# Kernel tuning notes

Hardware: AMD Instinct MI355X
Metric: run time of the kernel (lower is better)

The kernel has to match this reference:

```python
import jax, jax.numpy as jnp
import numpy as np

NUM_LEVELS = 16
F_PER_LEVEL = 2
LOG2_T = 19
TABLE_SIZE = 1 << LOG2_T  # 524288 entries per level
BASE_RES = 16
DESIRED_RES = 4096
PER_LEVEL_SCALE = np.exp(np.log(DESIRED_RES / BASE_RES) / (NUM_LEVELS - 1))
PRIMES = (np.uint32(1), np.uint32(2654435761), np.uint32(805459861))
N_POINTS = 4_194_304

# 8 corner offsets of the trilinear cell, bit i of corner index -> dim offset
_CORNERS = jnp.array([[(i >> d) & 1 for d in range(3)] for i in range(8)], dtype=jnp.float32)  # [8,3]


def hashgrid_encode(texc, table):
    """texc: [N,3] in [0,1]; table: [L, T, F]. Returns [N, L*F] (tcnn HashGrid math)."""
    feats = []
    for lvl in range(NUM_LEVELS):
        scale = float(np.exp2(lvl * np.log2(PER_LEVEL_SCALE)) * BASE_RES - 1.0)
        res = int(np.ceil(scale)) + 1
        pos = texc * scale + 0.5                    # [N,3]
        pg = jnp.floor(pos)
        frac = pos - pg                             # [N,3]
        corner = pg[:, None, :] + _CORNERS[None]    # [N,8,3]
        ci = corner.astype(jnp.uint32)
        # trilinear weights: prod over dims of frac (offset=1) or 1-frac (offset=0)
        w = jnp.prod(jnp.where(_CORNERS[None] == 1.0, frac[:, None, :], 1.0 - frac[:, None, :]), axis=-1)  # [N,8]
        if res ** 3 <= TABLE_SIZE:
            # dense level: index = x + y*res + z*res^2
            idx = ci[..., 0] + ci[..., 1] * jnp.uint32(res) + ci[..., 2] * jnp.uint32(res * res)
        else:
            # hashed level: spatial hash with xor of per-dim primes, mod 2^19
            idx = (ci[..., 0] * PRIMES[0]) ^ (ci[..., 1] * PRIMES[1]) ^ (ci[..., 2] * PRIMES[2])
            idx = idx & jnp.uint32(TABLE_SIZE - 1)
        g = table[lvl][idx.astype(jnp.int32)]       # [N,8,F] irregular gather
        feats.append(jnp.einsum('nc,ncf->nf', w, g))
    return jnp.concatenate(feats, axis=-1)          # [N, 32]


def setup_inputs() -> dict:
    key = jax.random.key(0)
    k0, k1, k2, k3, k4 = jax.random.split(key, 5)
    texc = jax.random.uniform(k0, (N_POINTS, 3), dtype=jnp.float32)
    # tcnn inits hashgrid params uniform in [-1e-4, 1e-4]
    table = (jax.random.uniform(k1, (NUM_LEVELS, TABLE_SIZE, F_PER_LEVEL), dtype=jnp.float32) * 2.0 - 1.0) * 1e-4
    # kaiming_uniform (relu) bound = sqrt(6/fan_in)
    def kaiming(k, shape):
        bound = float(np.sqrt(6.0 / shape[1]))
        return jax.random.uniform(k, shape, dtype=jnp.float32, minval=-bound, maxval=bound)
    W0 = kaiming(k2, (32, 32))
    W1 = kaiming(k3, (32, 32))
    W2 = kaiming(k4, (3, 32))
    return {"texc": texc, "table": table, "W0": W0, "W1": W1, "W2": W2}


def reference(texc, table, W0, W1, W2):
    enc = hashgrid_encode(texc, table)              # [N,32]
    h = jax.nn.relu(enc @ W0.T)
    h = jax.nn.relu(h @ W1.T)
    out = jax.nn.sigmoid(h @ W2.T)                  # [N,3]
    return out
```

## Files before the change

### kernel.cpp

```cpp
#include <hip/hip_runtime.h>
#include <math.h>

#define NUM_LEVELS 16
#define N_DENSE 5
#define N_HASH (NUM_LEVELS - N_DENSE)
#define TABLE_SIZE (1u << 19)
#define TMASK (TABLE_SIZE - 1u)

typedef float f32x4 __attribute__((ext_vector_type(4)));
typedef float f32x2 __attribute__((ext_vector_type(2)));
typedef short s16x8 __attribute__((ext_vector_type(8)));
typedef unsigned u32x2 __attribute__((ext_vector_type(2)));
typedef unsigned u32x4 __attribute__((ext_vector_type(4)));

struct HashParams { float scale[N_HASH]; };
struct DenseParams { float scale[N_DENSE]; unsigned res[N_DENSE]; };
struct AllParams { float scale[NUM_LEVELS]; unsigned res[NUM_LEVELS]; };

static __device__ __forceinline__ unsigned bf16_bits(float f) {
    const unsigned u = __builtin_bit_cast(unsigned, f);
    return (u + (0x7fffu + ((u >> 16) & 1u))) >> 16;
}
static __device__ __forceinline__ short bf16s(float f) { return (short)bf16_bits(f); }
static __device__ __forceinline__ float bflo(unsigned v) { return __builtin_bit_cast(float, v << 16); }
static __device__ __forceinline__ float bfhi(unsigned v) { return __builtin_bit_cast(float, v & 0xffff0000u); }

static __device__ __forceinline__ s16x8 packW8(const float* __restrict__ p) {
    const f32x4 a = *(const f32x4*)p;
    const f32x4 b = *(const f32x4*)(p + 4);
    s16x8 v;
    v[0] = bf16s(a.x); v[1] = bf16s(a.y); v[2] = bf16s(a.z); v[3] = bf16s(a.w);
    v[4] = bf16s(b.x); v[5] = bf16s(b.y); v[6] = bf16s(b.z); v[7] = bf16s(b.w);
    return v;
}
static __device__ __forceinline__ s16x8 packW8sig(const float* __restrict__ row, int q) {
    const f32x4 lo = *(const f32x4*)(row + 4 * q);
    const f32x4 hi = *(const f32x4*)(row + 16 + 4 * q);
    s16x8 v;
    v[0] = bf16s(lo.x); v[1] = bf16s(hi.x); v[2] = bf16s(lo.y); v[3] = bf16s(hi.y);
    v[4] = bf16s(lo.z); v[5] = bf16s(hi.z); v[6] = bf16s(lo.w); v[7] = bf16s(hi.w);
    return v;
}

__global__ __launch_bounds__(256) void cvt_table_kernel(
    const f32x4* __restrict__ src, u32x2* __restrict__ dst, int n2)
{
    const int i = blockIdx.x * 256 + threadIdx.x;
    if (i >= n2) return;
    const f32x4 g = __builtin_nontemporal_load(src + i);
    u32x2 o;
    o.x = bf16_bits(g.x) | (bf16_bits(g.y) << 16);
    o.y = bf16_bits(g.z) | (bf16_bits(g.w) << 16);
    dst[i] = o;
}

template <bool BT>
__global__ __launch_bounds__(256) void hashed_all_kernel(
    const float* __restrict__ texc,
    const float* __restrict__ tf,
    const unsigned* __restrict__ tb,
    unsigned* __restrict__ enc_ws,
    int n, int B, HashParams P)
{
    __shared__ float tst[768];
    const int tid = threadIdx.x;
    const unsigned lvl = blockIdx.x / (unsigned)B;
    const unsigned blk = blockIdx.x - lvl * (unsigned)B;
    const int i0 = (int)blk * 256;

    tst[tid]       = __builtin_nontemporal_load(texc + 3 * i0 + tid);
    tst[tid + 256] = __builtin_nontemporal_load(texc + 3 * i0 + tid + 256);
    tst[tid + 512] = __builtin_nontemporal_load(texc + 3 * i0 + tid + 512);
    __syncthreads();

    const float s = P.scale[lvl];
    const float tx = tst[3 * tid + 0], ty = tst[3 * tid + 1], tz = tst[3 * tid + 2];

    const float px = tx * s + 0.5f, py = ty * s + 0.5f, pz = tz * s + 0.5f;
    const float gx = floorf(px), gy = floorf(py), gz = floorf(pz);
    const float wx = px - gx, wy = py - gy, wz = pz - gz;
    const unsigned x0 = (unsigned)gx, y0 = (unsigned)gy, z0 = (unsigned)gz;

    const unsigned hy0 = y0 * 2654435761u, hy1 = (y0 + 1u) * 2654435761u;
    const unsigned hz0 = z0 * 805459861u,  hz1 = (z0 + 1u) * 805459861u;
    const unsigned hh[4] = { hy0 ^ hz0, hy1 ^ hz0, hy0 ^ hz1, hy1 ^ hz1 };
    const float wyz[4] = { (1.f - wy) * (1.f - wz), wy * (1.f - wz),
                           (1.f - wy) * wz,         wy * wz };
    const float wx0 = 1.f - wx, wx1 = wx;

    float f0 = 0.f, f1 = 0.f;

    if constexpr (BT) {
        const unsigned* tbl = tb + ((size_t)(N_DENSE + lvl) << 19);
        if ((x0 & 1u) == 0u) {
#pragma unroll
            for (int c = 0; c < 4; ++c) {
                const unsigned idx0 = (x0 ^ hh[c]) & TMASK;
                const u32x2 g = *(const u32x2*)(tbl + (idx0 & ~1u));
                const bool sw = (idx0 & 1u) != 0u;
                const unsigned ea = sw ? g.y : g.x;
                const unsigned eb = sw ? g.x : g.y;
                f0 += wyz[c] * (wx0 * bflo(ea) + wx1 * bflo(eb));
                f1 += wyz[c] * (wx0 * bfhi(ea) + wx1 * bfhi(eb));
            }
        } else {
#pragma unroll
            for (int c = 0; c < 4; ++c) {
                const unsigned ea = tbl[(x0 ^ hh[c]) & TMASK];
                const unsigned eb = tbl[((x0 + 1u) ^ hh[c]) & TMASK];
                f0 += wyz[c] * (wx0 * bflo(ea) + wx1 * bflo(eb));
                f1 += wyz[c] * (wx0 * bfhi(ea) + wx1 * bfhi(eb));
            }
        }
    } else {
        const float* tbl = tf + ((size_t)(N_DENSE + lvl) << 20);
        if ((x0 & 1u) == 0u) {
#pragma unroll
            for (int c = 0; c < 4; ++c) {
                const unsigned idx0 = (x0 ^ hh[c]) & TMASK;
                const f32x4 g = *(const f32x4*)(tbl + 2 * (size_t)(idx0 & ~1u));
                const bool hi = (idx0 & 1u) != 0u;
                const float g0x = hi ? g.z : g.x, g0y = hi ? g.w : g.y;
                const float g1x = hi ? g.x : g.z, g1y = hi ? g.y : g.w;
                f0 += wyz[c] * (wx0 * g0x + wx1 * g1x);
                f1 += wyz[c] * (wx0 * g0y + wx1 * g1y);
            }
        } else {
#pragma unroll
            for (int c = 0; c < 4; ++c) {
                const unsigned ia = (x0 ^ hh[c]) & TMASK;
                const unsigned ib = ((x0 + 1u) ^ hh[c]) & TMASK;
                const f32x2 ga = *(const f32x2*)(tbl + 2 * (size_t)ia);
                const f32x2 gb = *(const f32x2*)(tbl + 2 * (size_t)ib);
                f0 += wyz[c] * (wx0 * ga.x + wx1 * gb.x);
                f1 += wyz[c] * (wx0 * ga.y + wx1 * gb.y);
            }
        }
    }

    const unsigned packed = bf16_bits(f0) | (bf16_bits(f1) << 16);
    __builtin_nontemporal_store(packed, enc_ws + (size_t)lvl * n + (i0 + tid));
}

template <bool BT>
__global__ __launch_bounds__(256) void dense_mlp_kernel(
    const float* __restrict__ texc,
    const float* __restrict__ tf,
    const unsigned* __restrict__ tb,
    const unsigned* __restrict__ enc_ws,
    const float* __restrict__ W0,
    const float* __restrict__ W1,
    const float* __restrict__ W2,
    float* __restrict__ out,
    int n, DenseParams P)
{
    __shared__ float tst[768];
    __shared__ __align__(16) unsigned char slabs[4 * 64 * 80];
    const int tid = threadIdx.x;
    const int i0 = blockIdx.x * 256;

    tst[tid]       = __builtin_nontemporal_load(texc + 3 * i0 + tid);
    tst[tid + 256] = __builtin_nontemporal_load(texc + 3 * i0 + tid + 256);
    tst[tid + 512] = __builtin_nontemporal_load(texc + 3 * i0 + tid + 512);
    __syncthreads();

    const int i = i0 + tid;
    unsigned dd[16];

#pragma unroll
    for (int l = 0; l < N_HASH; ++l)
        dd[N_DENSE + l] = __builtin_nontemporal_load(enc_ws + (size_t)l * n + i);

    const float tx = tst[3 * tid + 0], ty = tst[3 * tid + 1], tz = tst[3 * tid + 2];

#pragma unroll
    for (int l = 0; l < N_DENSE; ++l) {
        const float s = P.scale[l];
        const unsigned res = P.res[l];
        const unsigned res2 = res * res;
        const float px = tx * s + 0.5f, py = ty * s + 0.5f, pz = tz * s + 0.5f;
        const float gx = floorf(px), gy = floorf(py), gz = floorf(pz);
        const float wx = px - gx, wy = py - gy, wz = pz - gz;
        const unsigned x0 = (unsigned)gx, y0 = (unsigned)gy, z0 = (unsigned)gz;
        const float wx0 = 1.f - wx, wx1 = wx;
        const float wyz[4] = { (1.f - wy) * (1.f - wz), wy * (1.f - wz),
                               (1.f - wy) * wz,         wy * wz };
        const unsigned base[4] = { y0 * res + z0 * res2, (y0 + 1u) * res + z0 * res2,
                                   y0 * res + (z0 + 1u) * res2,
                                   (y0 + 1u) * res + (z0 + 1u) * res2 };
        float f0 = 0.f, f1 = 0.f;
        if constexpr (BT) {
            const unsigned* tbl = tb + ((size_t)l << 19);
#pragma unroll
            for (int c = 0; c < 4; ++c) {
                const unsigned idx0 = x0 + base[c];
                unsigned ea, eb;
                if ((idx0 & 1u) == 0u) {
                    const u32x2 g = *(const u32x2*)(tbl + idx0);
                    ea = g.x; eb = g.y;
                } else {
                    ea = tbl[idx0]; eb = tbl[idx0 + 1u];
                }
                f0 += wyz[c] * (wx0 * bflo(ea) + wx1 * bflo(eb));
                f1 += wyz[c] * (wx0 * bfhi(ea) + wx1 * bfhi(eb));
            }
        } else {
            const float* tbl = tf + ((size_t)l << 20);
#pragma unroll
            for (int c = 0; c < 4; ++c) {
                const unsigned idx0 = x0 + base[c];
                if ((idx0 & 1u) == 0u) {
                    const f32x4 g = *(const f32x4*)(tbl + 2 * (size_t)idx0);
                    f0 += wyz[c] * (wx0 * g.x + wx1 * g.z);
                    f1 += wyz[c] * (wx0 * g.y + wx1 * g.w);
                } else {
                    const f32x2 ga = *(const f32x2*)(tbl + 2 * (size_t)idx0);
                    const f32x2 gb = *(const f32x2*)(tbl + 2 * (size_t)(idx0 + 1u));
                    f0 += wyz[c] * (wx0 * ga.x + wx1 * gb.x);
                    f1 += wyz[c] * (wx0 * ga.y + wx1 * gb.y);
                }
            }
        }
        dd[l] = bf16_bits(f0) | (bf16_bits(f1) << 16);
    }

    const int lane = tid & 63;
    const int wv = tid >> 6;
    const int c16 = lane & 15, q = lane >> 4;
    unsigned char* slabB = slabs + wv * (64 * 80);
    unsigned* slab = (unsigned*)slabB;

    *(u32x4*)(slabB + lane * 80 +  0) = (u32x4){ dd[0],  dd[1],  dd[2],  dd[3]  };
    *(u32x4*)(slabB + lane * 80 + 16) = (u32x4){ dd[4],  dd[5],  dd[6],  dd[7]  };
    *(u32x4*)(slabB + lane * 80 + 32) = (u32x4){ dd[8],  dd[9],  dd[10], dd[11] };
    *(u32x4*)(slabB + lane * 80 + 48) = (u32x4){ dd[12], dd[13], dd[14], dd[15] };

    const s16x8 b00 = packW8(W0 + c16 * 32 + 8 * q);
    const s16x8 b01 = packW8(W0 + (16 + c16) * 32 + 8 * q);
    const s16x8 b10 = packW8sig(W1 + c16 * 32, q);
    const s16x8 b11 = packW8sig(W1 + (16 + c16) * 32, q);
    const f32x4 zero4 = { 0.f, 0.f, 0.f, 0.f };

    f32x4 d0[4][2];
#pragma unroll
    for (int t = 0; t < 4; ++t) {
        const s16x8 a = *(const s16x8*)(slabB + (16 * t + c16) * 80 + 16 * q);
        d0[t][0] = __builtin_amdgcn_mfma_f32_16x16x32_bf16(a, b00, zero4, 0, 0, 0);
        d0[t][1] = __builtin_amdgcn_mfma_f32_16x16x32_bf16(a, b01, zero4, 0, 0, 0);
    }
#pragma unroll
    for (int t = 0; t < 4; ++t)
#pragma unroll
        for (int r = 0; r < 4; ++r) {
            const unsigned pk = bf16_bits(fmaxf(d0[t][0][r], 0.f)) |
                                (bf16_bits(fmaxf(d0[t][1][r], 0.f)) << 16);
            slab[(16 * t + 4 * q + r) * 20 + c16] = pk;
        }

    f32x4 d1[4][2];
#pragma unroll
    for (int t = 0; t < 4; ++t) {
        const s16x8 a = *(const s16x8*)(slabB + (16 * t + c16) * 80 + 16 * q);
        d1[t][0] = __builtin_amdgcn_mfma_f32_16x16x32_bf16(a, b10, zero4, 0, 0, 0);
        d1[t][1] = __builtin_amdgcn_mfma_f32_16x16x32_bf16(a, b11, zero4, 0, 0, 0);
    }
#pragma unroll
    for (int t = 0; t < 4; ++t)
#pragma unroll
        for (int r = 0; r < 4; ++r) {
            const unsigned pk = bf16_bits(fmaxf(d1[t][0][r], 0.f)) |
                                (bf16_bits(fmaxf(d1[t][1][r], 0.f)) << 16);
            slab[(16 * t + 4 * q + r) * 20 + c16] = pk;
        }

    float z0 = 0.f, z1 = 0.f, z2 = 0.f;
#pragma unroll
    for (int d = 0; d < 16; ++d) {
        const unsigned v = slab[lane * 20 + d];
        const float a0 = bflo(v), a1 = bfhi(v);
        z0 = fmaf(a0, W2[0 * 32 + d], fmaf(a1, W2[0 * 32 + 16 + d], z0));
        z1 = fmaf(a0, W2[1 * 32 + d], fmaf(a1, W2[1 * 32 + 16 + d], z1));
        z2 = fmaf(a0, W2[2 * 32 + d], fmaf(a1, W2[2 * 32 + 16 + d], z2));
    }
    out[3 * i + 0] = 1.f / (1.f + __expf(-z0));
    out[3 * i + 1] = 1.f / (1.f + __expf(-z1));
    out[3 * i + 2] = 1.f / (1.f + __expf(-z2));
}

__global__ __launch_bounds__(256) void mono_kernel(
    const float* __restrict__ texc, const float* __restrict__ table,
    const float* __restrict__ W0, const float* __restrict__ W1,
    const float* __restrict__ W2, float* __restrict__ out, int n, AllParams p)
{
    int i = blockIdx.x * 256 + threadIdx.x;
    if (i >= n) return;
    const float tx = texc[3 * i], ty = texc[3 * i + 1], tz = texc[3 * i + 2];
    float enc[2 * NUM_LEVELS];
#pragma unroll
    for (int l = 0; l < NUM_LEVELS; ++l) {
        const float s = p.scale[l];
        const unsigned res = p.res[l];
        const float px = tx * s + 0.5f, py = ty * s + 0.5f, pz = tz * s + 0.5f;
        const float gx = floorf(px), gy = floorf(py), gz = floorf(pz);
        const float wx = px - gx, wy = py - gy, wz = pz - gz;
        const unsigned x0 = (unsigned)gx, y0 = (unsigned)gy, z0 = (unsigned)gz;
        const float2* tbl = (const float2*)(table + ((size_t)l << 20));
        float f0 = 0.f, f1 = 0.f;
#pragma unroll
        for (int c = 0; c < 8; ++c) {
            const unsigned dx = c & 1u, dy = (c >> 1) & 1u, dz = (c >> 2) & 1u;
            const unsigned xi = x0 + dx, yi = y0 + dy, zi = z0 + dz;
            unsigned idx;
            if (l < N_DENSE) idx = xi + yi * res + zi * res * res;
            else idx = (xi ^ (yi * 2654435761u) ^ (zi * 805459861u)) & TMASK;
            const float2 g = tbl[idx];
            const float w = (dx ? wx : 1.f - wx) * (dy ? wy : 1.f - wy) *
                            (dz ? wz : 1.f - wz);
            f0 = fmaf(w, g.x, f0);
            f1 = fmaf(w, g.y, f1);
        }
        enc[2 * l] = f0;
        enc[2 * l + 1] = f1;
    }
    float h1[32];
#pragma unroll
    for (int j = 0; j < 32; ++j) {
        float acc = 0.f;
#pragma unroll
        for (int k = 0; k < 32; ++k) acc = fmaf(enc[k], W0[j * 32 + k], acc);
        h1[j] = fmaxf(acc, 0.f);
    }
    float h2[32];
#pragma unroll
    for (int j = 0; j < 32; ++j) {
        float acc = 0.f;
#pragma unroll
        for (int k = 0; k < 32; ++k) acc = fmaf(h1[k], W1[j * 32 + k], acc);
        h2[j] = fmaxf(acc, 0.f);
    }
#pragma unroll
    for (int j = 0; j < 3; ++j) {
        float acc = 0.f;
#pragma unroll
        for (int k = 0; k < 32; ++k) acc = fmaf(h2[k], W2[j * 32 + k], acc);
        out[3 * i + j] = 1.f / (1.f + __expf(-acc));
    }
}

extern "C" void kernel_launch(void* const* d_in, const int* in_sizes, int n_in,
                              void* d_out, int out_size, void* d_ws, size_t ws_size,
                              hipStream_t stream) {
    const float* texc  = (const float*)d_in[0];
    const float* table = (const float*)d_in[1];
    const float* W0    = (const float*)d_in[2];
    const float* W1    = (const float*)d_in[3];
    const float* W2    = (const float*)d_in[4];
    float* out = (float*)d_out;

    const int n = in_sizes[0] / 3;

    AllParams ap;
    const double log2pls = log(4096.0 / 16.0) / 15.0 / log(2.0);
    for (int l = 0; l < NUM_LEVELS; ++l) {
        const double sc = exp2((double)l * log2pls) * 16.0 - 1.0;
        ap.scale[l] = (float)sc;
        ap.res[l] = (unsigned)(ceil(sc) + 1.0);
    }
    HashParams hp;
    for (int l = 0; l < N_HASH; ++l) hp.scale[l] = ap.scale[l + N_DENSE];
    DenseParams dp;
    for (int l = 0; l < N_DENSE; ++l) { dp.scale[l] = ap.scale[l]; dp.res[l] = ap.res[l]; }

    const size_t enc_b = (size_t)N_HASH * (size_t)n * 4u;
    const size_t tbl_b = (size_t)NUM_LEVELS * TABLE_SIZE * 4u;

    if ((n % 256) == 0 && ws_size >= tbl_b + enc_b) {
        unsigned* bt = (unsigned*)d_ws;
        unsigned* enc_ws = bt + (size_t)NUM_LEVELS * TABLE_SIZE;
        const int B = n / 256;
        const int n2 = NUM_LEVELS * TABLE_SIZE / 2;
        cvt_table_kernel<<<(n2 + 255) / 256, 256, 0, stream>>>(
            (const f32x4*)table, (u32x2*)bt, n2);
        hashed_all_kernel<true><<<B * N_HASH, 256, 0, stream>>>(
            texc, table, bt, enc_ws, n, B, hp);
        dense_mlp_kernel<true><<<B, 256, 0, stream>>>(
            texc, table, bt, enc_ws, W0, W1, W2, out, n, dp);
    } else if ((n % 256) == 0 && ws_size >= enc_b) {
        unsigned* enc_ws = (unsigned*)d_ws;
        const int B = n / 256;
        hashed_all_kernel<false><<<B * N_HASH, 256, 0, stream>>>(
            texc, table, nullptr, enc_ws, n, B, hp);
        dense_mlp_kernel<false><<<B, 256, 0, stream>>>(
            texc, table, nullptr, enc_ws, W0, W1, W2, out, n, dp);
    } else {
        const int blocks = (n + 255) / 256;
        mono_kernel<<<blocks, 256, 0, stream>>>(texc, table, W0, W1, W2, out, n, ap);
    }
}
```

Measured before the change: 1.282 ms.

## Batch gathers for two points per thread and remove divergent branches

The hashed kernel now has each thread process two points, and every thread computes all corner indices before issuing all 16 paired 8-byte gathers at once. This raises memory-level parallelism and removes the even/odd x0 branch, at the cost of always issuing two loads per corner pair. The dense levels are restructured the same way, with gathers grouped across levels in two chunks, and the fp32-table fallback path is dropped. Register pressure rises and the grid for the hashed stage is halved.

```diff
diff --git a/kernel.cpp b/kernel.cpp
--- a/kernel.cpp
+++ b/kernel.cpp
@@ -8,7 +8,6 @@
 #define TMASK (TABLE_SIZE - 1u)
 
 typedef float f32x4 __attribute__((ext_vector_type(4)));
-typedef float f32x2 __attribute__((ext_vector_type(2)));
 typedef short s16x8 __attribute__((ext_vector_type(8)));
 typedef unsigned u32x2 __attribute__((ext_vector_type(2)));
 typedef unsigned u32x4 __attribute__((ext_vector_type(4)));
@@ -54,98 +53,81 @@
     dst[i] = o;
 }
 
-template <bool BT>
 __global__ __launch_bounds__(256) void hashed_all_kernel(
     const float* __restrict__ texc,
-    const float* __restrict__ tf,
     const unsigned* __restrict__ tb,
     unsigned* __restrict__ enc_ws,
-    int n, int B, HashParams P)
+    int n, int B2, HashParams P)
 {
-    __shared__ float tst[768];
+    __shared__ float tst[1536];
     const int tid = threadIdx.x;
-    const unsigned lvl = blockIdx.x / (unsigned)B;
-    const unsigned blk = blockIdx.x - lvl * (unsigned)B;
-    const int i0 = (int)blk * 256;
-
-    tst[tid]       = __builtin_nontemporal_load(texc + 3 * i0 + tid);
-    tst[tid + 256] = __builtin_nontemporal_load(texc + 3 * i0 + tid + 256);
-    tst[tid + 512] = __builtin_nontemporal_load(texc + 3 * i0 + tid + 512);
+    const unsigned lvl = blockIdx.x / (unsigned)B2;
+    const unsigned blk = blockIdx.x - lvl * (unsigned)B2;
+    const int i0 = (int)blk * 512;
+
+#pragma unroll
+    for (int j = 0; j < 6; ++j)
+        tst[tid + 256 * j] = __builtin_nontemporal_load(texc + 3 * i0 + 256 * j + tid);
     __syncthreads();
 
     const float s = P.scale[lvl];
-    const float tx = tst[3 * tid + 0], ty = tst[3 * tid + 1], tz = tst[3 * tid + 2];
-
-    const float px = tx * s + 0.5f, py = ty * s + 0.5f, pz = tz * s + 0.5f;
-    const float gx = floorf(px), gy = floorf(py), gz = floorf(pz);
-    const float wx = px - gx, wy = py - gy, wz = pz - gz;
-    const unsigned x0 = (unsigned)gx, y0 = (unsigned)gy, z0 = (unsigned)gz;
-
-    const unsigned hy0 = y0 * 2654435761u, hy1 = (y0 + 1u) * 2654435761u;
-    const unsigned hz0 = z0 * 805459861u,  hz1 = (z0 + 1u) * 805459861u;
-    const unsigned hh[4] = { hy0 ^ hz0, hy1 ^ hz0, hy0 ^ hz1, hy1 ^ hz1 };
-    const float wyz[4] = { (1.f - wy) * (1.f - wz), wy * (1.f - wz),
-                           (1.f - wy) * wz,         wy * wz };
-    const float wx0 = 1.f - wx, wx1 = wx;
-
-    float f0 = 0.f, f1 = 0.f;
-
-    if constexpr (BT) {
-        const unsigned* tbl = tb + ((size_t)(N_DENSE + lvl) << 19);
-        if ((x0 & 1u) == 0u) {
-#pragma unroll
-            for (int c = 0; c < 4; ++c) {
-                const unsigned idx0 = (x0 ^ hh[c]) & TMASK;
-                const u32x2 g = *(const u32x2*)(tbl + (idx0 & ~1u));
-                const bool sw = (idx0 & 1u) != 0u;
-                const unsigned ea = sw ? g.y : g.x;
-                const unsigned eb = sw ? g.x : g.y;
-                f0 += wyz[c] * (wx0 * bflo(ea) + wx1 * bflo(eb));
-                f1 += wyz[c] * (wx0 * bfhi(ea) + wx1 * bfhi(eb));
-            }
-        } else {
-#pragma unroll
-            for (int c = 0; c < 4; ++c) {
-                const unsigned ea = tbl[(x0 ^ hh[c]) & TMASK];
-                const unsigned eb = tbl[((x0 + 1u) ^ hh[c]) & TMASK];
-                f0 += wyz[c] * (wx0 * bflo(ea) + wx1 * bflo(eb));
-                f1 += wyz[c] * (wx0 * bfhi(ea) + wx1 * bfhi(eb));
-            }
-        }
-    } else {
-        const float* tbl = tf + ((size_t)(N_DENSE + lvl) << 20);
-        if ((x0 & 1u) == 0u) {
-#pragma unroll
-            for (int c = 0; c < 4; ++c) {
-                const unsigned idx0 = (x0 ^ hh[c]) & TMASK;
-                const f32x4 g = *(const f32x4*)(tbl + 2 * (size_t)(idx0 & ~1u));
-                const bool hi = (idx0 & 1u) != 0u;
-                const float g0x = hi ? g.z : g.x, g0y = hi ? g.w : g.y;
-                const float g1x = hi ? g.x : g.z, g1y = hi ? g.y : g.w;
-                f0 += wyz[c] * (wx0 * g0x + wx1 * g1x);
-                f1 += wyz[c] * (wx0 * g0y + wx1 * g1y);
-            }
-        } else {
-#pragma unroll
-            for (int c = 0; c < 4; ++c) {
-                const unsigned ia = (x0 ^ hh[c]) & TMASK;
-                const unsigned ib = ((x0 + 1u) ^ hh[c]) & TMASK;
-                const f32x2 ga = *(const f32x2*)(tbl + 2 * (size_t)ia);
-                const f32x2 gb = *(const f32x2*)(tbl + 2 * (size_t)ib);
-                f0 += wyz[c] * (wx0 * ga.x + wx1 * gb.x);
-                f1 += wyz[c] * (wx0 * ga.y + wx1 * gb.y);
-            }
-        }
-    }
-
-    const unsigned packed = bf16_bits(f0) | (bf16_bits(f1) << 16);
-    __builtin_nontemporal_store(packed, enc_ws + (size_t)lvl * n + (i0 + tid));
-}
-
-template <bool BT>
+    const unsigned* tbl = tb + ((size_t)(N_DENSE + lvl) << 19);
+
+    float wyzv[2][4], wxv[2][2];
+    unsigned pA[2][4], pB[2][4], sA[2][4], sB[2][4];
+
+#pragma unroll
+    for (int pp = 0; pp < 2; ++pp) {
+        const int t = tid + 256 * pp;
+        const float tx = tst[3 * t], ty = tst[3 * t + 1], tz = tst[3 * t + 2];
+        const float px = tx * s + 0.5f, py = ty * s + 0.5f, pz = tz * s + 0.5f;
+        const float gx = floorf(px), gy = floorf(py), gz = floorf(pz);
+        const float wx = px - gx, wy = py - gy, wz = pz - gz;
+        const unsigned x0 = (unsigned)gx, y0 = (unsigned)gy, z0 = (unsigned)gz;
+        const unsigned hy0 = y0 * 2654435761u, hy1 = (y0 + 1u) * 2654435761u;
+        const unsigned hz0 = z0 * 805459861u,  hz1 = (z0 + 1u) * 805459861u;
+        const unsigned hh[4] = { hy0 ^ hz0, hy1 ^ hz0, hy0 ^ hz1, hy1 ^ hz1 };
+        wyzv[pp][0] = (1.f - wy) * (1.f - wz);
+        wyzv[pp][1] = wy * (1.f - wz);
+        wyzv[pp][2] = (1.f - wy) * wz;
+        wyzv[pp][3] = wy * wz;
+        wxv[pp][0] = 1.f - wx; wxv[pp][1] = wx;
+#pragma unroll
+        for (int c = 0; c < 4; ++c) {
+            const unsigned ia = (x0 ^ hh[c]) & TMASK;
+            const unsigned ib = ((x0 + 1u) ^ hh[c]) & TMASK;
+            pA[pp][c] = ia & ~1u; sA[pp][c] = ia & 1u;
+            pB[pp][c] = ib & ~1u; sB[pp][c] = ib & 1u;
+        }
+    }
+
+    u32x2 gA[2][4], gB[2][4];
+#pragma unroll
+    for (int pp = 0; pp < 2; ++pp)
+#pragma unroll
+        for (int c = 0; c < 4; ++c) {
+            gA[pp][c] = *(const u32x2*)(tbl + pA[pp][c]);
+            gB[pp][c] = *(const u32x2*)(tbl + pB[pp][c]);
+        }
+
+#pragma unroll
+    for (int pp = 0; pp < 2; ++pp) {
+        float f0 = 0.f, f1 = 0.f;
+#pragma unroll
+        for (int c = 0; c < 4; ++c) {
+            const unsigned ea = sA[pp][c] ? gA[pp][c].y : gA[pp][c].x;
+            const unsigned eb = sB[pp][c] ? gB[pp][c].y : gB[pp][c].x;
+            f0 += wyzv[pp][c] * (wxv[pp][0] * bflo(ea) + wxv[pp][1] * bflo(eb));
+            f1 += wyzv[pp][c] * (wxv[pp][0] * bfhi(ea) + wxv[pp][1] * bfhi(eb));
+        }
+        const unsigned packed = bf16_bits(f0) | (bf16_bits(f1) << 16);
+        __builtin_nontemporal_store(packed,
+            enc_ws + (size_t)lvl * n + (i0 + tid + 256 * pp));
+    }
+}
+
 __global__ __launch_bounds__(256) void dense_mlp_kernel(
     const float* __restrict__ texc,
-    const float* __restrict__ tf,
     const unsigned* __restrict__ tb,
     const unsigned* __restrict__ enc_ws,
     const float* __restrict__ W0,
@@ -173,6 +155,8 @@
 
     const float tx = tst[3 * tid + 0], ty = tst[3 * tid + 1], tz = tst[3 * tid + 2];
 
+    float wyzd[N_DENSE][4], wx0d[N_DENSE], wx1d[N_DENSE];
+    unsigned iAd[N_DENSE][4], sAd[N_DENSE][4];
 #pragma unroll
     for (int l = 0; l < N_DENSE; ++l) {
         const float s = P.scale[l];
@@ -182,46 +166,48 @@
         const float gx = floorf(px), gy = floorf(py), gz = floorf(pz);
         const float wx = px - gx, wy = py - gy, wz = pz - gz;
         const unsigned x0 = (unsigned)gx, y0 = (unsigned)gy, z0 = (unsigned)gz;
-        const float wx0 = 1.f - wx, wx1 = wx;
-        const float wyz[4] = { (1.f - wy) * (1.f - wz), wy * (1.f - wz),
-                               (1.f - wy) * wz,         wy * wz };
-        const unsigned base[4] = { y0 * res + z0 * res2, (y0 + 1u) * res + z0 * res2,
-                                   y0 * res + (z0 + 1u) * res2,
-                                   (y0 + 1u) * res + (z0 + 1u) * res2 };
-        float f0 = 0.f, f1 = 0.f;
-        if constexpr (BT) {
-            const unsigned* tbl = tb + ((size_t)l << 19);
+        wx0d[l] = 1.f - wx; wx1d[l] = wx;
+        wyzd[l][0] = (1.f - wy) * (1.f - wz);
+        wyzd[l][1] = wy * (1.f - wz);
+        wyzd[l][2] = (1.f - wy) * wz;
+        wyzd[l][3] = wy * wz;
+        const unsigned b0 = y0 * res + z0 * res2;
+#pragma unroll
+        for (int c = 0; c < 4; ++c) {
+            const unsigned idx0 = x0 + b0 + (c & 1u) * res + (c >> 1) * res2;
+            iAd[l][c] = idx0 & ~1u;
+            sAd[l][c] = idx0 & 1u;
+        }
+    }
+
+#pragma unroll
+    for (int ch = 0; ch < 2; ++ch) {
+        const int l0 = ch ? 2 : 0, nl = ch ? 3 : 2;
+        u32x2 gA[3][4], gB[3][4];
+#pragma unroll
+        for (int k = 0; k < 3; ++k) {
+            if (k >= nl) break;
+            const unsigned* tbl = tb + ((size_t)(l0 + k) << 19);
 #pragma unroll
             for (int c = 0; c < 4; ++c) {
-                const unsigned idx0 = x0 + base[c];
-                unsigned ea, eb;
-                if ((idx0 & 1u) == 0u) {
-                    const u32x2 g = *(const u32x2*)(tbl + idx0);
-                    ea = g.x; eb = g.y;
-                } else {
-                    ea = tbl[idx0]; eb = tbl[idx0 + 1u];
-                }
-                f0 += wyz[c] * (wx0 * bflo(ea) + wx1 * bflo(eb));
-                f1 += wyz[c] * (wx0 * bfhi(ea) + wx1 * bfhi(eb));
+                gA[k][c] = *(const u32x2*)(tbl + iAd[l0 + k][c]);
+                gB[k][c] = *(const u32x2*)(tbl + ((iAd[l0 + k][c] + sAd[l0 + k][c] * 2u) & (TMASK & ~1u)));
             }
-        } else {
-            const float* tbl = tf + ((size_t)l << 20);
+        }
+#pragma unroll
+        for (int k = 0; k < 3; ++k) {
+            if (k >= nl) break;
+            const int l = l0 + k;
+            float f0 = 0.f, f1 = 0.f;
 #pragma unroll
             for (int c = 0; c < 4; ++c) {
-                const unsigned idx0 = x0 + base[c];
-                if ((idx0 & 1u) == 0u) {
-                    const f32x4 g = *(const f32x4*)(tbl + 2 * (size_t)idx0);
-                    f0 += wyz[c] * (wx0 * g.x + wx1 * g.z);
-                    f1 += wyz[c] * (wx0 * g.y + wx1 * g.w);
-                } else {
-                    const f32x2 ga = *(const f32x2*)(tbl + 2 * (size_t)idx0);
-                    const f32x2 gb = *(const f32x2*)(tbl + 2 * (size_t)(idx0 + 1u));
-                    f0 += wyz[c] * (wx0 * ga.x + wx1 * gb.x);
-                    f1 += wyz[c] * (wx0 * ga.y + wx1 * gb.y);
-                }
+                const unsigned ea = sAd[l][c] ? gA[k][c].y : gA[k][c].x;
+                const unsigned eb = sAd[l][c] ? gB[k][c].x : gB[k][c].y;
+                f0 += wyzd[l][c] * (wx0d[l] * bflo(ea) + wx1d[l] * bflo(eb));
+                f1 += wyzd[l][c] * (wx0d[l] * bfhi(ea) + wx1d[l] * bfhi(eb));
             }
-        }
-        dd[l] = bf16_bits(f0) | (bf16_bits(f1) << 16);
+            dd[l] = bf16_bits(f0) | (bf16_bits(f1) << 16);
+        }
     }
 
     const int lane = tid & 63;
@@ -366,32 +352,27 @@
         ap.scale[l] = (float)sc;
         ap.res[l] = (unsigned)(ceil(sc) + 1.0);
     }
-    HashParams hp;
-    for (int l = 0; l < N_HASH; ++l) hp.scale[l] = ap.scale[l + N_DENSE];
-    DenseParams dp;
-    for (int l = 0; l < N_DENSE; ++l) { dp.scale[l] = ap.scale[l]; dp.res[l] = ap.res[l]; }
 
     const size_t enc_b = (size_t)N_HASH * (size_t)n * 4u;
     const size_t tbl_b = (size_t)NUM_LEVELS * TABLE_SIZE * 4u;
 
-    if ((n % 256) == 0 && ws_size >= tbl_b + enc_b) {
+    if ((n % 512) == 0 && ws_size >= tbl_b + enc_b) {
+        HashParams hp;
+        for (int l = 0; l < N_HASH; ++l) hp.scale[l] = ap.scale[l + N_DENSE];
+        DenseParams dp;
+        for (int l = 0; l < N_DENSE; ++l) { dp.scale[l] = ap.scale[l]; dp.res[l] = ap.res[l]; }
+
         unsigned* bt = (unsigned*)d_ws;
         unsigned* enc_ws = bt + (size_t)NUM_LEVELS * TABLE_SIZE;
-        const int B = n / 256;
         const int n2 = NUM_LEVELS * TABLE_SIZE / 2;
         cvt_table_kernel<<<(n2 + 255) / 256, 256, 0, stream>>>(
             (const f32x4*)table, (u32x2*)bt, n2);
-        hashed_all_kernel<true><<<B * N_HASH, 256, 0, stream>>>(
-            texc, table, bt, enc_ws, n, B, hp);
-        dense_mlp_kernel<true><<<B, 256, 0, stream>>>(
-            texc, table, bt, enc_ws, W0, W1, W2, out, n, dp);
-    } else if ((n % 256) == 0 && ws_size >= enc_b) {
-        unsigned* enc_ws = (unsigned*)d_ws;
-        const int B = n / 256;
-        hashed_all_kernel<false><<<B * N_HASH, 256, 0, stream>>>(
-            texc, table, nullptr, enc_ws, n, B, hp);
-        dense_mlp_kernel<false><<<B, 256, 0, stream>>>(
-            texc, table, nullptr, enc_ws, W0, W1, W2, out, n, dp);
+
+        const int B2 = n / 512;
+        hashed_all_kernel<<<B2 * N_HASH, 256, 0, stream>>>(
+            texc, bt, enc_ws, n, B2, hp);
+        dense_mlp_kernel<<<n / 256, 256, 0, stream>>>(
+            texc, bt, enc_ws, W0, W1, W2, out, n, dp);
     } else {
         const int blocks = (n + 255) / 256;
         mono_kernel<<<blocks, 256, 0, stream>>>(texc, table, W0, W1, W2, out, n, ap);
```

Measured after the change: 1.416 ms. 10.5% more time.
